# Optimization experiments

Measured on AMD Instinct MI355X. Metric: run time of the kernel, lower is better.

Reference implementation:

```python
import jax, jax.numpy as jnp
import numpy as np

DIM = 1024
DEPTH = 4
HEADS = 16
DHEAD = 64
INNER = HEADS * DHEAD  # 1024
FF = 4 * DIM           # 4096
SCALE = DHEAD ** -0.5
LS_INIT = 0.1          # LayerScale init_eps for depth <= 18


def _layernorm(x, w, b):
    mu = jnp.mean(x, axis=-1, keepdims=True)
    var = jnp.mean((x - mu) ** 2, axis=-1, keepdims=True)
    return (x - mu) / jnp.sqrt(var + 1e-5) * w + b


def setup_inputs() -> dict:
    key = jax.random.key(0)
    ks = jax.random.split(key, 6)
    s = 0.02
    return {
        "x": jax.random.normal(ks[0], (2, 1024, DIM), dtype=jnp.float32),
        "ln1_w": jnp.ones((DEPTH, DIM), jnp.float32),
        "ln1_b": jnp.zeros((DEPTH, DIM), jnp.float32),
        "w_qkv": jax.random.normal(ks[1], (DEPTH, DIM, 3 * INNER), jnp.float32) * s,
        "w_out": jax.random.normal(ks[2], (DEPTH, INNER, DIM), jnp.float32) * s,
        "b_out": jnp.zeros((DEPTH, DIM), jnp.float32),
        "ls1": jnp.full((DEPTH, DIM), LS_INIT, jnp.float32),
        "ln2_w": jnp.ones((DEPTH, DIM), jnp.float32),
        "ln2_b": jnp.zeros((DEPTH, DIM), jnp.float32),
        "w_ff1": jax.random.normal(ks[3], (DEPTH, DIM, 2 * FF), jnp.float32) * s,
        "b_ff1": jnp.zeros((DEPTH, 2 * FF), jnp.float32),
        "w_ff2": jax.random.normal(ks[4], (DEPTH, FF, DIM), jnp.float32) * s,
        "b_ff2": jnp.zeros((DEPTH, DIM), jnp.float32),
        "ls2": jnp.full((DEPTH, DIM), LS_INIT, jnp.float32),
    }


def _block(x, p):
    (ln1w, ln1b, wqkv, wout, bout, ls1,
     ln2w, ln2b, wff1, bff1, wff2, bff2, ls2) = p
    b, n, _ = x.shape
    # --- PreNorm + Attention (non-causal, no mask) + LayerScale, residual ---
    h = _layernorm(x, ln1w, ln1b)
    qkv = h @ wqkv                                   # [b, n, 3*inner]
    q, k, v = jnp.split(qkv, 3, axis=-1)
    def heads(t):
        return t.reshape(b, n, HEADS, DHEAD).transpose(0, 2, 1, 3)  # b h n d
    q, k, v = heads(q) * SCALE, heads(k), heads(v)
    dots = jnp.einsum("bhid,bhjd->bhij", q, k)       # full O(n^2) scores
    attn = jax.nn.softmax(dots, axis=-1)
    o = jnp.einsum("bhij,bhjd->bhid", attn, v)
    o = o.transpose(0, 2, 1, 3).reshape(b, n, INNER)
    o = o @ wout + bout
    x = x + o * ls1
    # --- PreNorm + GEGLU FeedForward + LayerScale, residual ---
    h = _layernorm(x, ln2w, ln2b)
    u = h @ wff1 + bff1                              # [b, n, 2*FF]
    a, g = jnp.split(u, 2, axis=-1)
    ff = (a * jax.nn.gelu(g, approximate=False)) @ wff2 + bff2
    x = x + ff * ls2
    return x, None


def reference(x, ln1_w, ln1_b, w_qkv, w_out, b_out, ls1,
              ln2_w, ln2_b, w_ff1, b_ff1, w_ff2, b_ff2, ls2):
    ps = (ln1_w, ln1_b, w_qkv, w_out, b_out, ls1,
          ln2_w, ln2_b, w_ff1, b_ff1, w_ff2, b_ff2, ls2)
    out, _ = jax.lax.scan(_block, x, ps)
    return out
```

## Files before the change

kernel.cpp:

```cpp
#include <hip/hip_runtime.h>
#include <cstdint>
#include <cstddef>

typedef __bf16 bf16_t;
typedef __bf16 bf16x8 __attribute__((ext_vector_type(8)));
typedef __bf16 bf16x4 __attribute__((ext_vector_type(4)));
typedef float  f32x4  __attribute__((ext_vector_type(4)));

#define DEV __device__ __forceinline__

static constexpr int   BATCH = 2;
static constexpr int   NTOK  = 1024;
static constexpr int   DIM   = 1024;
static constexpr int   MROWS = BATCH * NTOK;
static constexpr float SCALE = 0.125f;

DEV void load_lds16(const bf16_t* g, bf16_t* s) {
  __builtin_amdgcn_global_load_lds(
      (const __attribute__((address_space(1))) void*)g,
      (__attribute__((address_space(3))) void*)s, 16, 0, 0);
}

DEV float wave_sum(float v) {
#pragma unroll
  for (int m = 1; m < 64; m <<= 1) v += __shfl_xor(v, m, 64);
  return v;
}
DEV float block_sum(float v, float* sb) {
  v = wave_sum(v);
  __syncthreads();
  if ((threadIdx.x & 63) == 0) sb[threadIdx.x >> 6] = v;
  __syncthreads();
  return sb[0] + sb[1] + sb[2] + sb[3];
}

template <int BM, int BN, int WR, int WC, int MODE>
__global__ __launch_bounds__(256) void gemm_bt(
    const bf16_t* __restrict__ A, long sA0, long sA1, int lda,
    const bf16_t* __restrict__ B, long sB0, long sB1, int ldb,
    void* __restrict__ Cv, long sC0, long sC1, int ldc,
    int K, float alpha, const float* __restrict__ bias,
    const float* __restrict__ ls) {
  constexpr int TM = BM / WR / 16;
  constexpr int TN = BN / WC / 16;
  __shared__ __attribute__((aligned(16))) bf16_t As[BM * 32];
  __shared__ __attribute__((aligned(16))) bf16_t Bs[BN * 32];

  const int tid  = threadIdx.x;
  const int lane = tid & 63, wave = tid >> 6;
  const int z  = blockIdx.z;
  const int zh = z >> 4, zl = z & 15;
  A += (size_t)zh * sA0 + (size_t)zl * sA1;
  B += (size_t)zh * sB0 + (size_t)zl * sB1;

  const int m0 = blockIdx.y * BM, n0 = blockIdx.x * BN;
  const int wm = (wave / WC) * (BM / WR);
  const int wn = (wave % WC) * (BN / WC);
  const int fm = lane & 15, quad = lane >> 4;

  f32x4 acc[TM][TN] = {};

  for (int k0 = 0; k0 < K; k0 += 32) {
#pragma unroll
    for (int c = tid; c < BM * 4; c += 256) {
      const int row = c >> 2, kc = (c & 3) << 3;
      load_lds16(A + (size_t)(m0 + row) * lda + k0 + kc, &As[c * 8]);
    }
#pragma unroll
    for (int c = tid; c < BN * 4; c += 256) {
      const int row = c >> 2, kc = (c & 3) << 3;
      load_lds16(B + (size_t)(n0 + row) * ldb + k0 + kc, &Bs[c * 8]);
    }
    __syncthreads();

    bf16x8 af[TM], bfr[TN];
#pragma unroll
    for (int i = 0; i < TM; ++i)
      af[i] = *(const bf16x8*)&As[(wm + i * 16 + fm) * 32 + quad * 8];
#pragma unroll
    for (int j = 0; j < TN; ++j)
      bfr[j] = *(const bf16x8*)&Bs[(wn + j * 16 + fm) * 32 + quad * 8];
#pragma unroll
    for (int i = 0; i < TM; ++i)
#pragma unroll
      for (int j = 0; j < TN; ++j)
        acc[i][j] = __builtin_amdgcn_mfma_f32_16x16x32_bf16(af[i], bfr[j],
                                                            acc[i][j], 0, 0, 0);
    __syncthreads();
  }

  const size_t coff = (size_t)zh * sC0 + (size_t)zl * sC1;
#pragma unroll
  for (int i = 0; i < TM; ++i) {
#pragma unroll
    for (int j = 0; j < TN; ++j) {
      const int col  = n0 + wn + j * 16 + fm;
      const int rowb = m0 + wm + i * 16 + quad * 4;
#pragma unroll
      for (int r = 0; r < 4; ++r) {
        const float  v   = acc[i][j][r];
        const size_t idx = coff + (size_t)(rowb + r) * ldc + col;
        if constexpr (MODE == 0) {
          ((bf16_t*)Cv)[idx] = (bf16_t)(v * alpha);
        } else if constexpr (MODE == 1) {
          ((bf16_t*)Cv)[idx] = (bf16_t)(v + bias[col]);
        } else {
          float* C = (float*)Cv;
          C[idx]   = C[idx] + (v + bias[col]) * ls[col];
        }
      }
    }
  }
}

__global__ __launch_bounds__(256) void flash_attn(
    const bf16_t* __restrict__ qkv,
    const bf16_t* __restrict__ vT,
    bf16_t* __restrict__ o) {
  constexpr int NT = 128;
  __shared__ __attribute__((aligned(16))) bf16_t Qs[2 * 64 * 32];
  __shared__ __attribute__((aligned(16))) bf16_t Ks[2 * NT * 32];
  __shared__ __attribute__((aligned(16))) bf16_t Vs[4 * 64 * 32];
  __shared__ __attribute__((aligned(16))) bf16_t Ps[4][4 * 16 * 32];

  const int tid = threadIdx.x, lane = tid & 63, wave = tid >> 6;
  const int fm = lane & 15, quad = lane >> 4;
  const int z = blockIdx.y, b = z >> 4, h = z & 15;
  const int q0 = blockIdx.x * 64;
  const bf16_t* qb  = qkv + (size_t)b * 1024 * 3072 + h * 64;
  const bf16_t* kb  = qb + 1024;
  const bf16_t* vtb = vT + (size_t)z * 64 * 1024;

  for (int c = tid; c < 512; c += 256) {
    const int kk = c >> 8, rr = (c >> 2) & 63, ii = c & 3;
    load_lds16(qb + (size_t)(q0 + rr) * 3072 + kk * 32 + ii * 8, &Qs[c * 8]);
  }
  __syncthreads();
  bf16x8 qf[2];
  qf[0] = *(const bf16x8*)&Qs[(wave * 16 + fm) * 32 + quad * 8];
  qf[1] = *(const bf16x8*)&Qs[64 * 32 + (wave * 16 + fm) * 32 + quad * 8];

  float mr[4], lr[4];
  f32x4 oacc[4];
#pragma unroll
  for (int r = 0; r < 4; ++r) { mr[r] = -1e30f; lr[r] = 0.f; }
#pragma unroll
  for (int t = 0; t < 4; ++t) oacc[t] = (f32x4){0.f, 0.f, 0.f, 0.f};

  for (int kv0 = 0; kv0 < 1024; kv0 += NT) {
    __syncthreads();
    for (int c = tid; c < NT * 8; c += 256) {
      const int kk = c >> 9, rr = (c >> 2) & 127, ii = c & 3;
      load_lds16(kb + (size_t)(kv0 + rr) * 3072 + kk * 32 + ii * 8, &Ks[c * 8]);
    }
    for (int c = tid; c < 1024; c += 256) {
      const int tc = c >> 8, rr = (c >> 2) & 63, ii = c & 3;
      load_lds16(vtb + (size_t)rr * 1024 + kv0 + tc * 32 + ii * 8, &Vs[c * 8]);
    }
    __syncthreads();

    f32x4 sc[8];
#pragma unroll
    for (int nt = 0; nt < 8; ++nt) {
      sc[nt] = (f32x4){0.f, 0.f, 0.f, 0.f};
#pragma unroll
      for (int kk = 0; kk < 2; ++kk) {
        const bf16x8 kf =
            *(const bf16x8*)&Ks[kk * NT * 32 + (nt * 16 + fm) * 32 + quad * 8];
        sc[nt] = __builtin_amdgcn_mfma_f32_16x16x32_bf16(qf[kk], kf, sc[nt],
                                                         0, 0, 0);
      }
    }
    float tmax[4] = {-1e30f, -1e30f, -1e30f, -1e30f};
#pragma unroll
    for (int nt = 0; nt < 8; ++nt)
#pragma unroll
      for (int r = 0; r < 4; ++r) {
        sc[nt][r] *= SCALE;
        tmax[r] = fmaxf(tmax[r], sc[nt][r]);
      }
#pragma unroll
    for (int m = 1; m < 16; m <<= 1)
#pragma unroll
      for (int r = 0; r < 4; ++r)
        tmax[r] = fmaxf(tmax[r], __shfl_xor(tmax[r], m, 64));
    float alpha[4], mn[4], ps[4];
#pragma unroll
    for (int r = 0; r < 4; ++r) {
      mn[r]    = fmaxf(mr[r], tmax[r]);
      alpha[r] = __expf(mr[r] - mn[r]);
      mr[r]    = mn[r];
      ps[r]    = 0.f;
    }
#pragma unroll
    for (int nt = 0; nt < 8; ++nt) {
      const int tcol = nt * 16 + fm, kk = tcol >> 5, tw = tcol & 31;
#pragma unroll
      for (int r = 0; r < 4; ++r) {
        const float p = __expf(sc[nt][r] - mn[r]);
        ps[r] += p;
        Ps[wave][kk * 512 + (quad * 4 + r) * 32 + tw] = (bf16_t)p;
      }
    }
#pragma unroll
    for (int m = 1; m < 16; m <<= 1)
#pragma unroll
      for (int r = 0; r < 4; ++r) ps[r] += __shfl_xor(ps[r], m, 64);
#pragma unroll
    for (int r = 0; r < 4; ++r) lr[r] = lr[r] * alpha[r] + ps[r];
#pragma unroll
    for (int t = 0; t < 4; ++t)
#pragma unroll
      for (int r = 0; r < 4; ++r) oacc[t][r] *= alpha[r];
    __builtin_amdgcn_s_waitcnt(0xC07F);
#pragma unroll
    for (int kk = 0; kk < 4; ++kk) {
      const bf16x8 af =
          *(const bf16x8*)&Ps[wave][kk * 512 + fm * 32 + quad * 8];
#pragma unroll
      for (int t = 0; t < 4; ++t) {
        const bf16x8 vf =
            *(const bf16x8*)&Vs[kk * 64 * 32 + (t * 16 + fm) * 32 + quad * 8];
        oacc[t] = __builtin_amdgcn_mfma_f32_16x16x32_bf16(af, vf, oacc[t],
                                                          0, 0, 0);
      }
    }
  }

  const size_t orow0 = (size_t)b * 1024 + q0 + wave * 16 + quad * 4;
#pragma unroll
  for (int t = 0; t < 4; ++t) {
    const int col = h * 64 + t * 16 + fm;
#pragma unroll
    for (int r = 0; r < 4; ++r)
      o[(orow0 + r) * 1024 + col] = (bf16_t)(oacc[t][r] / lr[r]);
  }
}

__global__ __launch_bounds__(256) void transpose_w(const float* __restrict__ W,
                                                   bf16_t* __restrict__ WT,
                                                   int K, int N) {
  __shared__ float t[32][33];
  const int n0 = blockIdx.x * 32, k0 = blockIdx.y * 32;
  const int tx = threadIdx.x & 31, ty = threadIdx.x >> 5;
#pragma unroll
  for (int s = 0; s < 4; ++s)
    t[ty + 8 * s][tx] = W[(size_t)(k0 + ty + 8 * s) * N + n0 + tx];
  __syncthreads();
#pragma unroll
  for (int s = 0; s < 4; ++s)
    WT[(size_t)(n0 + ty + 8 * s) * K + k0 + tx] = (bf16_t)t[tx][ty + 8 * s];
}

__global__ __launch_bounds__(256) void transpose_v(const bf16_t* __restrict__ qkv,
                                                   bf16_t* __restrict__ vT) {
  __shared__ bf16_t t[32][33];
  const int z = blockIdx.z, b = z >> 4, h = z & 15;
  const int d0 = blockIdx.y * 32, n0 = blockIdx.x * 32;
  const int tx = threadIdx.x & 31, ty = threadIdx.x >> 5;
  const bf16_t* src = qkv + (size_t)b * NTOK * 3072 + 2048 + h * 64;
#pragma unroll
  for (int s = 0; s < 4; ++s)
    t[ty + 8 * s][tx] = src[(size_t)(n0 + ty + 8 * s) * 3072 + d0 + tx];
  __syncthreads();
  bf16_t* dst = vT + (size_t)z * 64 * NTOK;
#pragma unroll
  for (int s = 0; s < 4; ++s)
    dst[(size_t)(d0 + ty + 8 * s) * NTOK + n0 + tx] = t[tx][ty + 8 * s];
}

__global__ __launch_bounds__(256) void ln_kernel(const float* __restrict__ x,
                                                 const float* __restrict__ w,
                                                 const float* __restrict__ b,
                                                 bf16_t* __restrict__ out) {
  __shared__ float sb[4];
  const int row = blockIdx.x, tid = threadIdx.x;
  const float4 v = ((const float4*)(x + (size_t)row * DIM))[tid];
  float s = v.x + v.y + v.z + v.w;
  s = block_sum(s, sb);
  const float mu = s * (1.f / DIM);
  const float dx = v.x - mu, dy = v.y - mu, dz = v.z - mu, dw = v.w - mu;
  float q = dx * dx + dy * dy + dz * dz + dw * dw;
  q = block_sum(q, sb);
  const float rstd = rsqrtf(q * (1.f / DIM) + 1e-5f);
  const float4 wv = ((const float4*)w)[tid];
  const float4 bv = ((const float4*)b)[tid];
  bf16x4 o;
  o[0] = (bf16_t)(dx * rstd * wv.x + bv.x);
  o[1] = (bf16_t)(dy * rstd * wv.y + bv.y);
  o[2] = (bf16_t)(dz * rstd * wv.z + bv.z);
  o[3] = (bf16_t)(dw * rstd * wv.w + bv.w);
  ((bf16x4*)(out + (size_t)row * DIM))[tid] = o;
}

__global__ __launch_bounds__(256) void geglu_kernel(const bf16_t* __restrict__ u,
                                                    bf16_t* __restrict__ ff) {
  const int g   = blockIdx.x * 256 + threadIdx.x;
  const int row = g >> 10, cg = (g & 1023) * 4;
  const bf16x4 av = *(const bf16x4*)(u + (size_t)row * 8192 + cg);
  const bf16x4 gv = *(const bf16x4*)(u + (size_t)row * 8192 + 4096 + cg);
  bf16x4 o;
#pragma unroll
  for (int c = 0; c < 4; ++c) {
    const float gx = (float)gv[c];
    const float ge = 0.5f * gx * (1.f + erff(gx * 0.70710678118654752f));
    o[c] = (bf16_t)((float)av[c] * ge);
  }
  *(bf16x4*)(ff + (size_t)row * 4096 + cg) = o;
}

extern "C" void kernel_launch(void* const* d_in, const int* in_sizes, int n_in,
                              void* d_out, int out_size, void* d_ws,
                              size_t ws_size, hipStream_t stream) {
  const float* x_in = (const float*)d_in[0];
  const float* ln1w = (const float*)d_in[1];
  const float* ln1b = (const float*)d_in[2];
  const float* wqkv = (const float*)d_in[3];
  const float* wout = (const float*)d_in[4];
  const float* bout = (const float*)d_in[5];
  const float* ls1  = (const float*)d_in[6];
  const float* ln2w = (const float*)d_in[7];
  const float* ln2b = (const float*)d_in[8];
  const float* wff1 = (const float*)d_in[9];
  const float* bff1 = (const float*)d_in[10];
  const float* wff2 = (const float*)d_in[11];
  const float* bff2 = (const float*)d_in[12];
  const float* ls2  = (const float*)d_in[13];
  float*       xout = (float*)d_out;

  char*   ws     = (char*)d_ws;
  bf16_t* wqkvT  = (bf16_t*)ws; ws += (size_t)3072 * 1024 * 2;
  bf16_t* woutT  = (bf16_t*)ws; ws += (size_t)1024 * 1024 * 2;
  bf16_t* wff1T  = (bf16_t*)ws; ws += (size_t)8192 * 1024 * 2;
  bf16_t* wff2T  = (bf16_t*)ws; ws += (size_t)1024 * 4096 * 2;
  bf16_t* h_bf   = (bf16_t*)ws; ws += (size_t)MROWS * 1024 * 2;
  bf16_t* qkv_bf = (bf16_t*)ws; ws += (size_t)MROWS * 3072 * 2;
  bf16_t* o_bf   = (bf16_t*)ws; ws += (size_t)MROWS * 1024 * 2;
  bf16_t* vT     = (bf16_t*)ws; ws += (size_t)32 * 64 * 1024 * 2;
  bf16_t* u_bf   = (bf16_t*)ws; ws += (size_t)MROWS * 8192 * 2;
  bf16_t* ff_bf  = (bf16_t*)ws; ws += (size_t)MROWS * 4096 * 2;
  if (ws_size < (size_t)(ws - (char*)d_ws)) return;

  hipMemcpyAsync(xout, x_in, (size_t)MROWS * DIM * 4,
                 hipMemcpyDeviceToDevice, stream);

  for (int l = 0; l < 4; ++l) {
    transpose_w<<<dim3(3072 / 32, 1024 / 32), 256, 0, stream>>>(
        wqkv + (size_t)l * 1024 * 3072, wqkvT, 1024, 3072);
    transpose_w<<<dim3(1024 / 32, 1024 / 32), 256, 0, stream>>>(
        wout + (size_t)l * 1024 * 1024, woutT, 1024, 1024);
    transpose_w<<<dim3(8192 / 32, 1024 / 32), 256, 0, stream>>>(
        wff1 + (size_t)l * 1024 * 8192, wff1T, 1024, 8192);
    transpose_w<<<dim3(1024 / 32, 4096 / 32), 256, 0, stream>>>(
        wff2 + (size_t)l * 4096 * 1024, wff2T, 4096, 1024);

    ln_kernel<<<MROWS, 256, 0, stream>>>(xout, ln1w + l * 1024,
                                         ln1b + l * 1024, h_bf);
    gemm_bt<128, 128, 2, 2, 0><<<dim3(24, 16, 1), 256, 0, stream>>>(
        h_bf, 0, 0, 1024, wqkvT, 0, 0, 1024, qkv_bf, 0, 0, 3072, 1024, 1.f,
        nullptr, nullptr);
    transpose_v<<<dim3(32, 2, 32), 256, 0, stream>>>(qkv_bf, vT);
    flash_attn<<<dim3(16, 32), 256, 0, stream>>>(qkv_bf, vT, o_bf);
    gemm_bt<64, 128, 1, 4, 2><<<dim3(8, 32, 1), 256, 0, stream>>>(
        o_bf, 0, 0, 1024, woutT, 0, 0, 1024, xout, 0, 0, 1024, 1024, 1.f,
        bout + l * 1024, ls1 + l * 1024);

    ln_kernel<<<MROWS, 256, 0, stream>>>(xout, ln2w + l * 1024,
                                         ln2b + l * 1024, h_bf);
    gemm_bt<128, 128, 2, 2, 1><<<dim3(64, 16, 1), 256, 0, stream>>>(
        h_bf, 0, 0, 1024, wff1T, 0, 0, 1024, u_bf, 0, 0, 8192, 1024, 1.f,
        bff1 + l * 8192, nullptr);
    geglu_kernel<<<8192, 256, 0, stream>>>(u_bf, ff_bf);
    gemm_bt<64, 128, 1, 4, 2><<<dim3(8, 32, 1), 256, 0, stream>>>(
        ff_bf, 0, 0, 4096, wff2T, 0, 0, 4096, xout, 0, 0, 1024, 4096, 1.f,
        bff2 + l * 1024, ls2 + l * 1024);
  }
}
```

Measured before the change: 1.226 ms.

## Fuse GEGLU into FF1 GEMM, batch weight transposes, split-K out GEMMs, register-resident P

Fuses the GEGLU activation into the FF1 GEMM epilogue by computing value and gate tiles together, which removes the 32MB intermediate u buffer and the separate geglu kernel. Weight transposes for all four layers now run in one batched launch each before the layer loop. The output and FF2 GEMMs use split-K with atomicAdd into the residual, adding bias only on the last split. The Q scale is folded into the QKV GEMM epilogue. Flash attention computes S transposed so P stays in registers and feeds a 16x16x16 MFMA without an LDS round trip. In exchange, the atomics make accumulation order nondeterministic and the workspace for transposed weights grows fourfold.

After: 1.331 ms. 1.09x slower.

```diff
diff --git a/kernel.cpp b/kernel.cpp
--- a/kernel.cpp
+++ b/kernel.cpp
@@ -6,6 +6,7 @@
 typedef __bf16 bf16x8 __attribute__((ext_vector_type(8)));
 typedef __bf16 bf16x4 __attribute__((ext_vector_type(4)));
 typedef float  f32x4  __attribute__((ext_vector_type(4)));
+typedef short  s16x4  __attribute__((ext_vector_type(4)));
 
 #define DEV __device__ __forceinline__
 
@@ -90,6 +91,7 @@
   }
 
   const size_t coff = (size_t)zh * sC0 + (size_t)zl * sC1;
+  const bool last_z = (zl + 1 == (int)gridDim.z);
 #pragma unroll
   for (int i = 0; i < TM; ++i) {
 #pragma unroll
@@ -101,13 +103,92 @@
         const float  v   = acc[i][j][r];
         const size_t idx = coff + (size_t)(rowb + r) * ldc + col;
         if constexpr (MODE == 0) {
-          ((bf16_t*)Cv)[idx] = (bf16_t)(v * alpha);
+          ((bf16_t*)Cv)[idx] = (bf16_t)(col < 1024 ? v * alpha : v);
         } else if constexpr (MODE == 1) {
           ((bf16_t*)Cv)[idx] = (bf16_t)(v + bias[col]);
         } else {
-          float* C = (float*)Cv;
-          C[idx]   = C[idx] + (v + bias[col]) * ls[col];
+          const float bb = (bias && last_z) ? bias[col] : 0.f;
+          atomicAdd(&((float*)Cv)[idx], (v + bb) * ls[col]);
         }
+      }
+    }
+  }
+}
+
+template <int BM, int BN>
+__global__ __launch_bounds__(256) void gemm_ff1_geglu(
+    const bf16_t* __restrict__ A, int lda,
+    const bf16_t* __restrict__ BT,
+    bf16_t* __restrict__ ff,
+    const float* __restrict__ bias,
+    int K) {
+  constexpr int WR = 2, WC = 2;
+  constexpr int TM = BM / WR / 16;
+  constexpr int TN = BN / WC / 16;
+  __shared__ __attribute__((aligned(16))) bf16_t As[BM * 32];
+  __shared__ __attribute__((aligned(16))) bf16_t Bas[BN * 32];
+  __shared__ __attribute__((aligned(16))) bf16_t Bgs[BN * 32];
+
+  const int tid  = threadIdx.x;
+  const int lane = tid & 63, wave = tid >> 6;
+  const int m0 = blockIdx.y * BM, n0 = blockIdx.x * BN;
+  const int wm = (wave / WC) * (BM / WR);
+  const int wn = (wave % WC) * (BN / WC);
+  const int fm = lane & 15, quad = lane >> 4;
+
+  const bf16_t* Ba = BT + (size_t)n0 * K;
+  const bf16_t* Bg = BT + (size_t)(n0 + 4096) * K;
+
+  f32x4 acca[TM][TN] = {}, accg[TM][TN] = {};
+
+  for (int k0 = 0; k0 < K; k0 += 32) {
+#pragma unroll
+    for (int c = tid; c < BM * 4; c += 256) {
+      const int row = c >> 2, kc = (c & 3) << 3;
+      load_lds16(A + (size_t)(m0 + row) * lda + k0 + kc, &As[c * 8]);
+    }
+#pragma unroll
+    for (int c = tid; c < BN * 4; c += 256) {
+      const int row = c >> 2, kc = (c & 3) << 3;
+      load_lds16(Ba + (size_t)row * K + k0 + kc, &Bas[c * 8]);
+      load_lds16(Bg + (size_t)row * K + k0 + kc, &Bgs[c * 8]);
+    }
+    __syncthreads();
+
+    bf16x8 af[TM], ba[TN], bg[TN];
+#pragma unroll
+    for (int i = 0; i < TM; ++i)
+      af[i] = *(const bf16x8*)&As[(wm + i * 16 + fm) * 32 + quad * 8];
+#pragma unroll
+    for (int j = 0; j < TN; ++j) {
+      ba[j] = *(const bf16x8*)&Bas[(wn + j * 16 + fm) * 32 + quad * 8];
+      bg[j] = *(const bf16x8*)&Bgs[(wn + j * 16 + fm) * 32 + quad * 8];
+    }
+#pragma unroll
+    for (int i = 0; i < TM; ++i)
+#pragma unroll
+      for (int j = 0; j < TN; ++j) {
+        acca[i][j] = __builtin_amdgcn_mfma_f32_16x16x32_bf16(af[i], ba[j],
+                                                             acca[i][j], 0, 0, 0);
+        accg[i][j] = __builtin_amdgcn_mfma_f32_16x16x32_bf16(af[i], bg[j],
+                                                             accg[i][j], 0, 0, 0);
+      }
+    __syncthreads();
+  }
+
+#pragma unroll
+  for (int i = 0; i < TM; ++i) {
+#pragma unroll
+    for (int j = 0; j < TN; ++j) {
+      const int col  = n0 + wn + j * 16 + fm;
+      const int rowb = m0 + wm + i * 16 + quad * 4;
+      const float ab = bias[col], gb = bias[col + 4096];
+#pragma unroll
+      for (int r = 0; r < 4; ++r) {
+        const float a  = acca[i][j][r] + ab;
+        const float g  = accg[i][j][r] + gb;
+        const float ge = 0.5f * g * (1.f + erff(g * 0.70710678118654752f));
+        ff[(size_t)(rowb + r) * 4096 + col] = (bf16_t)(a * ge);
       }
     }
   }
@@ -121,7 +202,6 @@
   __shared__ __attribute__((aligned(16))) bf16_t Qs[2 * 64 * 32];
   __shared__ __attribute__((aligned(16))) bf16_t Ks[2 * NT * 32];
   __shared__ __attribute__((aligned(16))) bf16_t Vs[4 * 64 * 32];
-  __shared__ __attribute__((aligned(16))) bf16_t Ps[4][4 * 16 * 32];
 
   const int tid = threadIdx.x, lane = tid & 63, wave = tid >> 6;
   const int fm = lane & 15, quad = lane >> 4;
@@ -140,12 +220,8 @@
   qf[0] = *(const bf16x8*)&Qs[(wave * 16 + fm) * 32 + quad * 8];
   qf[1] = *(const bf16x8*)&Qs[64 * 32 + (wave * 16 + fm) * 32 + quad * 8];
 
-  float mr[4], lr[4];
-  f32x4 oacc[4];
-#pragma unroll
-  for (int r = 0; r < 4; ++r) { mr[r] = -1e30f; lr[r] = 0.f; }
-#pragma unroll
-  for (int t = 0; t < 4; ++t) oacc[t] = (f32x4){0.f, 0.f, 0.f, 0.f};
+  float mr = -1e30f, lr = 0.f;
+  f32x4 oacc[4] = {};
 
   for (int kv0 = 0; kv0 < 1024; kv0 += NT) {
     __syncthreads();
@@ -159,81 +235,75 @@
     }
     __syncthreads();
 
-    f32x4 sc[8];
+    f32x4 st[8];
 #pragma unroll
     for (int nt = 0; nt < 8; ++nt) {
-      sc[nt] = (f32x4){0.f, 0.f, 0.f, 0.f};
+      st[nt] = (f32x4){0.f, 0.f, 0.f, 0.f};
 #pragma unroll
       for (int kk = 0; kk < 2; ++kk) {
         const bf16x8 kf =
             *(const bf16x8*)&Ks[kk * NT * 32 + (nt * 16 + fm) * 32 + quad * 8];
-        sc[nt] = __builtin_amdgcn_mfma_f32_16x16x32_bf16(qf[kk], kf, sc[nt],
+        st[nt] = __builtin_amdgcn_mfma_f32_16x16x32_bf16(kf, qf[kk], st[nt],
                                                          0, 0, 0);
       }
     }
-    float tmax[4] = {-1e30f, -1e30f, -1e30f, -1e30f};
+    float mx = st[0][0];
 #pragma unroll
     for (int nt = 0; nt < 8; ++nt)
 #pragma unroll
+      for (int r = 0; r < 4; ++r) mx = fmaxf(mx, st[nt][r]);
+    mx = fmaxf(mx, __shfl_xor(mx, 16, 64));
+    mx = fmaxf(mx, __shfl_xor(mx, 32, 64));
+    const float mn = fmaxf(mr, mx);
+    const float al = __expf(mr - mn);
+    mr = mn;
+    float ps = 0.f;
+    s16x4 pf[8];
+#pragma unroll
+    for (int nt = 0; nt < 8; ++nt) {
+      bf16x4 pv;
+#pragma unroll
       for (int r = 0; r < 4; ++r) {
-        sc[nt][r] *= SCALE;
-        tmax[r] = fmaxf(tmax[r], sc[nt][r]);
-      }
-#pragma unroll
-    for (int m = 1; m < 16; m <<= 1)
-#pragma unroll
-      for (int r = 0; r < 4; ++r)
-        tmax[r] = fmaxf(tmax[r], __shfl_xor(tmax[r], m, 64));
-    float alpha[4], mn[4], ps[4];
-#pragma unroll
-    for (int r = 0; r < 4; ++r) {
-      mn[r]    = fmaxf(mr[r], tmax[r]);
-      alpha[r] = __expf(mr[r] - mn[r]);
-      mr[r]    = mn[r];
-      ps[r]    = 0.f;
-    }
+        const float p = __expf(st[nt][r] - mn);
+        ps += p;
+        pv[r] = (bf16_t)p;
+      }
+      pf[nt] = __builtin_bit_cast(s16x4, pv);
+    }
+    ps += __shfl_xor(ps, 16, 64);
+    ps += __shfl_xor(ps, 32, 64);
+    lr = lr * al + ps;
+    float alr[4];
+#pragma unroll
+    for (int r = 0; r < 4; ++r) alr[r] = __shfl(al, quad * 4 + r, 64);
+#pragma unroll
+    for (int t = 0; t < 4; ++t)
+#pragma unroll
+      for (int r = 0; r < 4; ++r) oacc[t][r] *= alr[r];
 #pragma unroll
     for (int nt = 0; nt < 8; ++nt) {
-      const int tcol = nt * 16 + fm, kk = tcol >> 5, tw = tcol & 31;
-#pragma unroll
-      for (int r = 0; r < 4; ++r) {
-        const float p = __expf(sc[nt][r] - mn[r]);
-        ps[r] += p;
-        Ps[wave][kk * 512 + (quad * 4 + r) * 32 + tw] = (bf16_t)p;
-      }
-    }
-#pragma unroll
-    for (int m = 1; m < 16; m <<= 1)
-#pragma unroll
-      for (int r = 0; r < 4; ++r) ps[r] += __shfl_xor(ps[r], m, 64);
-#pragma unroll
-    for (int r = 0; r < 4; ++r) lr[r] = lr[r] * alpha[r] + ps[r];
-#pragma unroll
-    for (int t = 0; t < 4; ++t)
-#pragma unroll
-      for (int r = 0; r < 4; ++r) oacc[t][r] *= alpha[r];
-    __builtin_amdgcn_s_waitcnt(0xC07F);
-#pragma unroll
-    for (int kk = 0; kk < 4; ++kk) {
-      const bf16x8 af =
-          *(const bf16x8*)&Ps[wave][kk * 512 + fm * 32 + quad * 8];
+      const int tok = nt * 16 + quad * 4;
+      const int tc = tok >> 5, tin = tok & 31;
 #pragma unroll
       for (int t = 0; t < 4; ++t) {
-        const bf16x8 vf =
-            *(const bf16x8*)&Vs[kk * 64 * 32 + (t * 16 + fm) * 32 + quad * 8];
-        oacc[t] = __builtin_amdgcn_mfma_f32_16x16x32_bf16(af, vf, oacc[t],
-                                                          0, 0, 0);
-      }
-    }
-  }
-
+        const bf16x4 vv =
+            *(const bf16x4*)&Vs[tc * 2048 + (t * 16 + fm) * 32 + tin];
+        oacc[t] = __builtin_amdgcn_mfma_f32_16x16x16bf16_1k(
+            pf[nt], __builtin_bit_cast(s16x4, vv), oacc[t], 0, 0, 0);
+      }
+    }
+  }
+
+  float linv[4];
+#pragma unroll
+  for (int r = 0; r < 4; ++r) linv[r] = 1.f / __shfl(lr, quad * 4 + r, 64);
   const size_t orow0 = (size_t)b * 1024 + q0 + wave * 16 + quad * 4;
 #pragma unroll
   for (int t = 0; t < 4; ++t) {
     const int col = h * 64 + t * 16 + fm;
 #pragma unroll
     for (int r = 0; r < 4; ++r)
-      o[(orow0 + r) * 1024 + col] = (bf16_t)(oacc[t][r] / lr[r]);
+      o[(orow0 + r) * 1024 + col] = (bf16_t)(oacc[t][r] * linv[r]);
   }
 }
 
@@ -241,6 +311,8 @@
                                                    bf16_t* __restrict__ WT,
                                                    int K, int N) {
   __shared__ float t[32][33];
+  W  += (size_t)blockIdx.z * K * N;
+  WT += (size_t)blockIdx.z * K * N;
   const int n0 = blockIdx.x * 32, k0 = blockIdx.y * 32;
   const int tx = threadIdx.x & 31, ty = threadIdx.x >> 5;
 #pragma unroll
@@ -293,22 +365,6 @@
   ((bf16x4*)(out + (size_t)row * DIM))[tid] = o;
 }
 
-__global__ __launch_bounds__(256) void geglu_kernel(const bf16_t* __restrict__ u,
-                                                    bf16_t* __restrict__ ff) {
-  const int g   = blockIdx.x * 256 + threadIdx.x;
-  const int row = g >> 10, cg = (g & 1023) * 4;
-  const bf16x4 av = *(const bf16x4*)(u + (size_t)row * 8192 + cg);
-  const bf16x4 gv = *(const bf16x4*)(u + (size_t)row * 8192 + 4096 + cg);
-  bf16x4 o;
-#pragma unroll
-  for (int c = 0; c < 4; ++c) {
-    const float gx = (float)gv[c];
-    const float ge = 0.5f * gx * (1.f + erff(gx * 0.70710678118654752f));
-    o[c] = (bf16_t)((float)av[c] * ge);
-  }
-  *(bf16x4*)(ff + (size_t)row * 4096 + cg) = o;
-}
-
 extern "C" void kernel_launch(void* const* d_in, const int* in_sizes, int n_in,
                               void* d_out, int out_size, void* d_ws,
                               size_t ws_size, hipStream_t stream) {
@@ -329,50 +385,48 @@
   float*       xout = (float*)d_out;
 
   char*   ws     = (char*)d_ws;
-  bf16_t* wqkvT  = (bf16_t*)ws; ws += (size_t)3072 * 1024 * 2;
-  bf16_t* woutT  = (bf16_t*)ws; ws += (size_t)1024 * 1024 * 2;
-  bf16_t* wff1T  = (bf16_t*)ws; ws += (size_t)8192 * 1024 * 2;
-  bf16_t* wff2T  = (bf16_t*)ws; ws += (size_t)1024 * 4096 * 2;
+  bf16_t* wqkvT  = (bf16_t*)ws; ws += (size_t)4 * 3072 * 1024 * 2;
+  bf16_t* woutT  = (bf16_t*)ws; ws += (size_t)4 * 1024 * 1024 * 2;
+  bf16_t* wff1T  = (bf16_t*)ws; ws += (size_t)4 * 8192 * 1024 * 2;
+  bf16_t* wff2T  = (bf16_t*)ws; ws += (size_t)4 * 1024 * 4096 * 2;
   bf16_t* h_bf   = (bf16_t*)ws; ws += (size_t)MROWS * 1024 * 2;
   bf16_t* qkv_bf = (bf16_t*)ws; ws += (size_t)MROWS * 3072 * 2;
   bf16_t* o_bf   = (bf16_t*)ws; ws += (size_t)MROWS * 1024 * 2;
   bf16_t* vT     = (bf16_t*)ws; ws += (size_t)32 * 64 * 1024 * 2;
-  bf16_t* u_bf   = (bf16_t*)ws; ws += (size_t)MROWS * 8192 * 2;
   bf16_t* ff_bf  = (bf16_t*)ws; ws += (size_t)MROWS * 4096 * 2;
   if (ws_size < (size_t)(ws - (char*)d_ws)) return;
 
   hipMemcpyAsync(xout, x_in, (size_t)MROWS * DIM * 4,
                  hipMemcpyDeviceToDevice, stream);
 
+  transpose_w<<<dim3(96, 32, 4), 256, 0, stream>>>(wqkv, wqkvT, 1024, 3072);
+  transpose_w<<<dim3(32, 32, 4), 256, 0, stream>>>(wout, woutT, 1024, 1024);
+  transpose_w<<<dim3(256, 32, 4), 256, 0, stream>>>(wff1, wff1T, 1024, 8192);
+  transpose_w<<<dim3(32, 128, 4), 256, 0, stream>>>(wff2, wff2T, 4096, 1024);
+
   for (int l = 0; l < 4; ++l) {
-    transpose_w<<<dim3(3072 / 32, 1024 / 32), 256, 0, stream>>>(
-        wqkv + (size_t)l * 1024 * 3072, wqkvT, 1024, 3072);
-    transpose_w<<<dim3(1024 / 32, 1024 / 32), 256, 0, stream>>>(
-        wout + (size_t)l * 1024 * 1024, woutT, 1024, 1024);
-    transpose_w<<<dim3(8192 / 32, 1024 / 32), 256, 0, stream>>>(
-        wff1 + (size_t)l * 1024 * 8192, wff1T, 1024, 8192);
-    transpose_w<<<dim3(1024 / 32, 4096 / 32), 256, 0, stream>>>(
-        wff2 + (size_t)l * 4096 * 1024, wff2T, 4096, 1024);
+    const bf16_t* wqkvTl = wqkvT + (size_t)l * 3072 * 1024;
+    const bf16_t* woutTl = woutT + (size_t)l * 1024 * 1024;
+    const bf16_t* wff1Tl = wff1T + (size_t)l * 8192 * 1024;
+    const bf16_t* wff2Tl = wff2T + (size_t)l * 4096 * 1024;
 
     ln_kernel<<<MROWS, 256, 0, stream>>>(xout, ln1w + l * 1024,
                                          ln1b + l * 1024, h_bf);
-    gemm_bt<128, 128, 2, 2, 0><<<dim3(24, 16, 1), 256, 0, stream>>>(
-        h_bf, 0, 0, 1024, wqkvT, 0, 0, 1024, qkv_bf, 0, 0, 3072, 1024, 1.f,
-        nullptr, nullptr);
+    gemm_bt<64, 128, 1, 4, 0><<<dim3(24, 32, 1), 256, 0, stream>>>(
+        h_bf, 0, 0, 1024, wqkvTl, 0, 0, 1024, qkv_bf, 0, 0, 3072, 1024,
+        SCALE, nullptr, nullptr);
     transpose_v<<<dim3(32, 2, 32), 256, 0, stream>>>(qkv_bf, vT);
     flash_attn<<<dim3(16, 32), 256, 0, stream>>>(qkv_bf, vT, o_bf);
-    gemm_bt<64, 128, 1, 4, 2><<<dim3(8, 32, 1), 256, 0, stream>>>(
-        o_bf, 0, 0, 1024, woutT, 0, 0, 1024, xout, 0, 0, 1024, 1024, 1.f,
-        bout + l * 1024, ls1 + l * 1024);
+    gemm_bt<64, 128, 1, 4, 2><<<dim3(8, 32, 2), 256, 0, stream>>>(
+        o_bf, 0, 512, 1024, woutTl, 0, 512, 1024, xout, 0, 0, 1024, 512,
+        1.f, bout + l * 1024, ls1 + l * 1024);
 
     ln_kernel<<<MROWS, 256, 0, stream>>>(xout, ln2w + l * 1024,
                                          ln2b + l * 1024, h_bf);
-    gemm_bt<128, 128, 2, 2, 1><<<dim3(64, 16, 1), 256, 0, stream>>>(
-        h_bf, 0, 0, 1024, wff1T, 0, 0, 1024, u_bf, 0, 0, 8192, 1024, 1.f,
-        bff1 + l * 8192, nullptr);
-    geglu_kernel<<<8192, 256, 0, stream>>>(u_bf, ff_bf);
-    gemm_bt<64, 128, 1, 4, 2><<<dim3(8, 32, 1), 256, 0, stream>>>(
-        ff_bf, 0, 0, 4096, wff2T, 0, 0, 4096, xout, 0, 0, 1024, 4096, 1.f,
-        bff2 + l * 1024, ls2 + l * 1024);
-  }
-}
+    gemm_ff1_geglu<128, 128><<<dim3(32, 16), 256, 0, stream>>>(
+        h_bf, 1024, wff1Tl, ff_bf, bff1 + l * 8192, 1024);
+    gemm_bt<64, 128, 1, 4, 2><<<dim3(8, 32, 2), 256, 0, stream>>>(
+        ff_bf, 0, 2048, 4096, wff2Tl, 0, 2048, 4096, xout, 0, 0, 1024, 2048,
+        1.f, bff2 + l * 1024, ls2 + l * 1024);
+  }
+}
```
